# Kernel optimization log

Hardware: AMD Instinct MI355X
Metric: run time of the kernel (lower is better)

The kernel has to match this reference:

```python
import jax, jax.numpy as jnp
import numpy as np

ALPHA = 0.1
D_K = 24  # hardcoded in the original module


def adj_tanh(x, a):
    # exact formula from the original: (e^m - e^-m) / (e^m + e^-m)
    m = a * x
    em, enm = jnp.exp(m), jnp.exp(-m)
    return (em - enm) / (em + enm)


def setup_inputs() -> dict:
    key = jax.random.key(0)
    kq, kk, kv = jax.random.split(key, 3)
    B, H, S, D = 2, 8, 2048, D_K
    Q = jax.random.normal(kq, (B, H, S, D), dtype=jnp.float32)
    K = jax.random.normal(kk, (B, H, S, D), dtype=jnp.float32)
    V = jax.random.normal(kv, (B, H, S, D), dtype=jnp.float32)
    attn_mask = jnp.zeros((B, H, S, S), dtype=jnp.bool_)
    return {"Q": Q, "K": K, "V": V, "attn_mask": attn_mask}


def reference(Q, K, V, attn_mask):
    scale = jnp.float32(1.0 / np.sqrt(D_K))
    # [B,H,S,S] scores
    scores = jnp.einsum("bhqd,bhkd->bhqk", Q, K) * scale
    attn = adj_tanh(scores, ALPHA)
    # NOTE: original uses non-in-place `attn.masked_fill(attn_mask, 0.0)` and
    # discards the result, so the mask has no effect. Replicated faithfully.
    context = jnp.einsum("bhqk,bhkd->bhqd", attn, V)
    return context
```

## Files before the change

### kernel.cpp

```cpp
#include <hip/hip_runtime.h>


#define S_LEN 2048
#define HD 24
#define CMUL 0.02041241452319315f

typedef short short8 __attribute__((ext_vector_type(8)));
typedef float f32x4 __attribute__((ext_vector_type(4)));
typedef unsigned int uint4v __attribute__((ext_vector_type(4)));

static __device__ __forceinline__ unsigned int f2bf_u(float f) {
  unsigned int u = __float_as_uint(f);
  u += 0x7FFFu + ((u >> 16) & 1u);
  return u >> 16;
}

static __device__ __forceinline__ float tanh_fast(float m) {
  m = fminf(fmaxf(m, -9.f), 9.f);
  float t = __expf(2.f * m);
  return (t - 1.f) * __builtin_amdgcn_rcpf(t + 1.f);
}

static __device__ __forceinline__ short8 load_frag24(const float* rowp, int lg) {
  short8 f = {0, 0, 0, 0, 0, 0, 0, 0};
  if (lg < 3) {
    const float4 x = *reinterpret_cast<const float4*>(rowp);
    const float4 y = *reinterpret_cast<const float4*>(rowp + 4);
    f[0] = (short)f2bf_u(x.x); f[1] = (short)f2bf_u(x.y);
    f[2] = (short)f2bf_u(x.z); f[3] = (short)f2bf_u(x.w);
    f[4] = (short)f2bf_u(y.x); f[5] = (short)f2bf_u(y.y);
    f[6] = (short)f2bf_u(y.z); f[7] = (short)f2bf_u(y.w);
  }
  return f;
}

extern "C" __global__ __launch_bounds__(256, 2) void attn_tanh_fused(
    const float* __restrict__ Qg, const float* __restrict__ Kg,
    const float* __restrict__ Vg, float* __restrict__ Og) {
  __shared__ float part[4][32][32];

  const int tid = threadIdx.x;
  const int w   = tid >> 6;
  const int l   = tid & 63;
  const int lr  = l & 15;
  const int lg  = l >> 4;
  const int bh  = blockIdx.y;
  const int q0  = blockIdx.x * 32;

  const float* Qb = Qg + bh * S_LEN * HD;
  const float* Kb = Kg + bh * S_LEN * HD;
  const float* Vb = Vg + bh * S_LEN * HD;

  short8 qf[2];
#pragma unroll
  for (int sub = 0; sub < 2; ++sub)
    qf[sub] = load_frag24(Qb + (q0 + sub * 16 + lr) * HD + lg * 8, lg);

  const f32x4 zero4 = {0.f, 0.f, 0.f, 0.f};
  f32x4 acc[2][2];
#pragma unroll
  for (int i = 0; i < 2; ++i)
#pragma unroll
    for (int j = 0; j < 2; ++j) acc[i][j] = zero4;

  const int kv0  = w * (S_LEN / 4);
  const int srcA = lr + ((lg & 1) << 5);
  const int srcB = srcA + 16;
  const bool hi  = (lg >> 1) != 0;

#pragma unroll 2
  for (int kt = kv0; kt < kv0 + S_LEN / 4; kt += 32) {
    short8 kf0 = load_frag24(Kb + (kt + lr) * HD + lg * 8, lg);
    short8 kf1 = load_frag24(Kb + (kt + 16 + lr) * HD + lg * 8, lg);

    short8 vf0, vf1;
    {
      const float* vp = Vb + (kt + lg * 8) * HD;
      const int c1 = lr + 16;
#pragma unroll
      for (int j = 0; j < 8; ++j) {
        vf0[j] = (short)f2bf_u(vp[j * HD + lr]);
        vf1[j] = (short)(c1 < HD ? f2bf_u(vp[j * HD + c1]) : 0u);
      }
    }

#pragma unroll
    for (int sub = 0; sub < 2; ++sub) {
      f32x4 s0 = __builtin_amdgcn_mfma_f32_16x16x32_bf16(kf0, qf[sub], zero4, 0, 0, 0);
      f32x4 s1 = __builtin_amdgcn_mfma_f32_16x16x32_bf16(kf1, qf[sub], zero4, 0, 0, 0);

      unsigned int u0 = f2bf_u(tanh_fast(CMUL * s0[0])) | (f2bf_u(tanh_fast(CMUL * s0[1])) << 16);
      unsigned int u1 = f2bf_u(tanh_fast(CMUL * s0[2])) | (f2bf_u(tanh_fast(CMUL * s0[3])) << 16);
      unsigned int u2 = f2bf_u(tanh_fast(CMUL * s1[0])) | (f2bf_u(tanh_fast(CMUL * s1[1])) << 16);
      unsigned int u3 = f2bf_u(tanh_fast(CMUL * s1[2])) | (f2bf_u(tanh_fast(CMUL * s1[3])) << 16);

      unsigned int a0A = (unsigned int)__shfl((int)u0, srcA, 64);
      unsigned int a1A = (unsigned int)__shfl((int)u1, srcA, 64);
      unsigned int a2A = (unsigned int)__shfl((int)u2, srcA, 64);
      unsigned int a3A = (unsigned int)__shfl((int)u3, srcA, 64);
      unsigned int a0B = (unsigned int)__shfl((int)u0, srcB, 64);
      unsigned int a1B = (unsigned int)__shfl((int)u1, srcB, 64);
      unsigned int a2B = (unsigned int)__shfl((int)u2, srcB, 64);
      unsigned int a3B = (unsigned int)__shfl((int)u3, srcB, 64);

      uint4v pw;
      pw[0] = hi ? a2A : a0A;
      pw[1] = hi ? a3A : a1A;
      pw[2] = hi ? a2B : a0B;
      pw[3] = hi ? a3B : a1B;
      short8 pa = __builtin_bit_cast(short8, pw);

      acc[sub][0] = __builtin_amdgcn_mfma_f32_16x16x32_bf16(pa, vf0, acc[sub][0], 0, 0, 0);
      acc[sub][1] = __builtin_amdgcn_mfma_f32_16x16x32_bf16(pa, vf1, acc[sub][1], 0, 0, 0);
    }
  }

#pragma unroll
  for (int sub = 0; sub < 2; ++sub)
#pragma unroll
    for (int ct = 0; ct < 2; ++ct)
#pragma unroll
      for (int r = 0; r < 4; ++r)
        part[w][sub * 16 + lg * 4 + r][ct * 16 + lr] = acc[sub][ct][r];

  __syncthreads();

  float* Ob = Og + bh * S_LEN * HD + q0 * HD;
  for (int idx = tid; idx < 32 * HD; idx += 256) {
    const int row = idx / HD;
    const int d = idx - row * HD;
    Ob[idx] = part[0][row][d] + part[1][row][d] + part[2][row][d] + part[3][row][d];
  }
}

extern "C" void kernel_launch(void* const* d_in, const int* in_sizes, int n_in,
                              void* d_out, int out_size, void* d_ws, size_t ws_size,
                              hipStream_t stream) {
  (void)in_sizes; (void)n_in; (void)d_ws; (void)ws_size; (void)out_size;
  const float* Q = (const float*)d_in[0];
  const float* K = (const float*)d_in[1];
  const float* V = (const float*)d_in[2];
  float* O = (float*)d_out;

  dim3 grid(S_LEN / 32, 16);
  attn_tanh_fused<<<grid, 256, 0, stream>>>(Q, K, V, O);
}
```

Before: 374.9 us.

## Preconvert Q/K to padded bf16, pre-transpose V, fold scale into Q

```diff
diff --git a/kernel.cpp b/kernel.cpp
--- a/kernel.cpp
+++ b/kernel.cpp
@@ -1,42 +1,90 @@
 #include <hip/hip_runtime.h>
+#include <hip/hip_bf16.h>
 
 
 #define S_LEN 2048
 #define HD 24
 #define CMUL 0.02041241452319315f
+#define C2 (2.0f * CMUL * 1.4426950408889634f)
 
 typedef short short8 __attribute__((ext_vector_type(8)));
 typedef float f32x4 __attribute__((ext_vector_type(4)));
 typedef unsigned int uint4v __attribute__((ext_vector_type(4)));
 
-static __device__ __forceinline__ unsigned int f2bf_u(float f) {
-  unsigned int u = __float_as_uint(f);
-  u += 0x7FFFu + ((u >> 16) & 1u);
-  return u >> 16;
+static __device__ __forceinline__ unsigned int pack_bf16(float a, float b) {
+  __hip_bfloat162 h = __float22bfloat162_rn(float2{a, b});
+  unsigned int u;
+  __builtin_memcpy(&u, &h, 4);
+  return u;
 }
 
-static __device__ __forceinline__ float tanh_fast(float m) {
-  m = fminf(fmaxf(m, -9.f), 9.f);
-  float t = __expf(2.f * m);
-  return (t - 1.f) * __builtin_amdgcn_rcpf(t + 1.f);
+static __device__ __forceinline__ float exp2_fast(float x) {
+#if __has_builtin(__builtin_amdgcn_exp2f)
+  return __builtin_amdgcn_exp2f(x);
+#else
+  return exp2f(x);
+#endif
 }
 
-static __device__ __forceinline__ short8 load_frag24(const float* rowp, int lg) {
-  short8 f = {0, 0, 0, 0, 0, 0, 0, 0};
-  if (lg < 3) {
-    const float4 x = *reinterpret_cast<const float4*>(rowp);
-    const float4 y = *reinterpret_cast<const float4*>(rowp + 4);
-    f[0] = (short)f2bf_u(x.x); f[1] = (short)f2bf_u(x.y);
-    f[2] = (short)f2bf_u(x.z); f[3] = (short)f2bf_u(x.w);
-    f[4] = (short)f2bf_u(y.x); f[5] = (short)f2bf_u(y.y);
-    f[6] = (short)f2bf_u(y.z); f[7] = (short)f2bf_u(y.w);
+static __device__ __forceinline__ float tanh1(float m2) {
+  float t = exp2_fast(m2);
+  float r = __builtin_amdgcn_rcpf(t + 1.f);
+  return __builtin_fmaf(-2.f, r, 1.f);
+}
+
+extern "C" __global__ __launch_bounds__(256) void convert_pad_rows(
+    const float* __restrict__ src, unsigned int* __restrict__ dst, float scale) {
+  const int row = blockIdx.x * 256 + threadIdx.x;
+  const float* s = src + row * HD;
+  float v[24];
+#pragma unroll
+  for (int i = 0; i < 6; ++i) {
+    float4 x = *reinterpret_cast<const float4*>(s + i * 4);
+    v[i * 4 + 0] = x.x; v[i * 4 + 1] = x.y; v[i * 4 + 2] = x.z; v[i * 4 + 3] = x.w;
   }
-  return f;
+  uint4v o[4];
+#pragma unroll
+  for (int i = 0; i < 12; ++i)
+    ((unsigned int*)o)[i] = pack_bf16(v[2 * i] * scale, v[2 * i + 1] * scale);
+  o[3][0] = 0; o[3][1] = 0; o[3][2] = 0; o[3][3] = 0;
+  uint4v* d = reinterpret_cast<uint4v*>(dst + row * 16);
+  d[0] = o[0]; d[1] = o[1]; d[2] = o[2]; d[3] = o[3];
+}
+
+extern "C" __global__ __launch_bounds__(256) void transpose_v(
+    const float* __restrict__ V, unsigned short* __restrict__ Vt) {
+  __shared__ float lds[128][25];
+  const int t = threadIdx.x;
+  const int bh = blockIdx.y;
+  const int kv0 = blockIdx.x * 128;
+  const float* Vb = V + (bh * S_LEN + kv0) * HD;
+  {
+    const int r = t >> 1, c0 = (t & 1) * 12;
+    const float* p = Vb + r * HD + c0;
+#pragma unroll
+    for (int i = 0; i < 3; ++i) {
+      float4 x = *reinterpret_cast<const float4*>(p + i * 4);
+      lds[r][c0 + i * 4 + 0] = x.x; lds[r][c0 + i * 4 + 1] = x.y;
+      lds[r][c0 + i * 4 + 2] = x.z; lds[r][c0 + i * 4 + 3] = x.w;
+    }
+  }
+  __syncthreads();
+  const int d = t >> 3, seg = (t & 7) * 16;
+  unsigned int ob[8];
+#pragma unroll
+  for (int k = 0; k < 8; ++k) {
+    float a = (d < HD) ? lds[seg + 2 * k][d] : 0.f;
+    float b = (d < HD) ? lds[seg + 2 * k + 1][d] : 0.f;
+    ob[k] = pack_bf16(a, b);
+  }
+  uint4v* dst = reinterpret_cast<uint4v*>(Vt + (bh * 32 + d) * S_LEN + kv0 + seg);
+  dst[0] = *reinterpret_cast<uint4v*>(&ob[0]);
+  dst[1] = *reinterpret_cast<uint4v*>(&ob[4]);
 }
 
 extern "C" __global__ __launch_bounds__(256, 2) void attn_tanh_fused(
-    const float* __restrict__ Qg, const float* __restrict__ Kg,
-    const float* __restrict__ Vg, float* __restrict__ Og) {
+    const unsigned short* __restrict__ QsU, const unsigned short* __restrict__ KsU,
+    const unsigned short* __restrict__ VtU, float* __restrict__ Og) {
   __shared__ float part[4][32][32];
 
   const int tid = threadIdx.x;
@@ -47,14 +95,13 @@
   const int bh  = blockIdx.y;
   const int q0  = blockIdx.x * 32;
 
-  const float* Qb = Qg + bh * S_LEN * HD;
-  const float* Kb = Kg + bh * S_LEN * HD;
-  const float* Vb = Vg + bh * S_LEN * HD;
+  const short8* Qp = reinterpret_cast<const short8*>(QsU) + bh * (S_LEN * 4);
+  const short8* Kp = reinterpret_cast<const short8*>(KsU) + bh * (S_LEN * 4);
+  const short8* Vp = reinterpret_cast<const short8*>(VtU) + bh * (32 * 256);
 
   short8 qf[2];
-#pragma unroll
-  for (int sub = 0; sub < 2; ++sub)
-    qf[sub] = load_frag24(Qb + (q0 + sub * 16 + lr) * HD + lg * 8, lg);
+  qf[0] = Qp[(q0 + lr) * 4 + lg];
+  qf[1] = Qp[(q0 + 16 + lr) * 4 + lg];
 
   const f32x4 zero4 = {0.f, 0.f, 0.f, 0.f};
   f32x4 acc[2][2];
@@ -70,29 +117,20 @@
 
 #pragma unroll 2
   for (int kt = kv0; kt < kv0 + S_LEN / 4; kt += 32) {
-    short8 kf0 = load_frag24(Kb + (kt + lr) * HD + lg * 8, lg);
-    short8 kf1 = load_frag24(Kb + (kt + 16 + lr) * HD + lg * 8, lg);
-
-    short8 vf0, vf1;
-    {
-      const float* vp = Vb + (kt + lg * 8) * HD;
-      const int c1 = lr + 16;
-#pragma unroll
-      for (int j = 0; j < 8; ++j) {
-        vf0[j] = (short)f2bf_u(vp[j * HD + lr]);
-        vf1[j] = (short)(c1 < HD ? f2bf_u(vp[j * HD + c1]) : 0u);
-      }
-    }
+    short8 kf0 = Kp[(kt + lr) * 4 + lg];
+    short8 kf1 = Kp[(kt + 16 + lr) * 4 + lg];
+    short8 vf0 = Vp[lr * 256 + (kt >> 3) + lg];
+    short8 vf1 = Vp[(16 + lr) * 256 + (kt >> 3) + lg];
 
 #pragma unroll
     for (int sub = 0; sub < 2; ++sub) {
       f32x4 s0 = __builtin_amdgcn_mfma_f32_16x16x32_bf16(kf0, qf[sub], zero4, 0, 0, 0);
       f32x4 s1 = __builtin_amdgcn_mfma_f32_16x16x32_bf16(kf1, qf[sub], zero4, 0, 0, 0);
 
-      unsigned int u0 = f2bf_u(tanh_fast(CMUL * s0[0])) | (f2bf_u(tanh_fast(CMUL * s0[1])) << 16);
-      unsigned int u1 = f2bf_u(tanh_fast(CMUL * s0[2])) | (f2bf_u(tanh_fast(CMUL * s0[3])) << 16);
-      unsigned int u2 = f2bf_u(tanh_fast(CMUL * s1[0])) | (f2bf_u(tanh_fast(CMUL * s1[1])) << 16);
-      unsigned int u3 = f2bf_u(tanh_fast(CMUL * s1[2])) | (f2bf_u(tanh_fast(CMUL * s1[3])) << 16);
+      unsigned int u0 = pack_bf16(tanh1(s0[0]), tanh1(s0[1]));
+      unsigned int u1 = pack_bf16(tanh1(s0[2]), tanh1(s0[3]));
+      unsigned int u2 = pack_bf16(tanh1(s1[0]), tanh1(s1[1]));
+      unsigned int u3 = pack_bf16(tanh1(s1[2]), tanh1(s1[3]));
 
       unsigned int a0A = (unsigned int)__shfl((int)u0, srcA, 64);
       unsigned int a1A = (unsigned int)__shfl((int)u1, srcA, 64);
@@ -108,7 +146,8 @@
       pw[1] = hi ? a3A : a1A;
       pw[2] = hi ? a2B : a0B;
       pw[3] = hi ? a3B : a1B;
-      short8 pa = __builtin_bit_cast(short8, pw);
+      short8 pa;
+      __builtin_memcpy(&pa, &pw, 16);
 
       acc[sub][0] = __builtin_amdgcn_mfma_f32_16x16x32_bf16(pa, vf0, acc[sub][0], 0, 0, 0);
       acc[sub][1] = __builtin_amdgcn_mfma_f32_16x16x32_bf16(pa, vf1, acc[sub][1], 0, 0, 0);
@@ -136,12 +175,20 @@
 extern "C" void kernel_launch(void* const* d_in, const int* in_sizes, int n_in,
                               void* d_out, int out_size, void* d_ws, size_t ws_size,
                               hipStream_t stream) {
-  (void)in_sizes; (void)n_in; (void)d_ws; (void)ws_size; (void)out_size;
+  (void)in_sizes; (void)n_in; (void)out_size; (void)ws_size;
   const float* Q = (const float*)d_in[0];
   const float* K = (const float*)d_in[1];
   const float* V = (const float*)d_in[2];
   float* O = (float*)d_out;
 
+  unsigned short* Qs = (unsigned short*)d_ws;
+  unsigned short* Ks = Qs + 16 * S_LEN * 32;
+  unsigned short* Vt = Ks + 16 * S_LEN * 32;
+
+  convert_pad_rows<<<dim3(16 * S_LEN / 256), 256, 0, stream>>>(Q, (unsigned int*)Qs, C2);
+  convert_pad_rows<<<dim3(16 * S_LEN / 256), 256, 0, stream>>>(K, (unsigned int*)Ks, 1.0f);
+  transpose_v<<<dim3(S_LEN / 128, 16), 256, 0, stream>>>(V, Vt);
+
   dim3 grid(S_LEN / 32, 16);
-  attn_tanh_fused<<<grid, 256, 0, stream>>>(Q, K, V, O);
+  attn_tanh_fused<<<grid, 256, 0, stream>>>(Qs, Ks, Vt, O);
 }
```

New measurement: 331.7 us. 1.13x faster.
